# Kernel tuning notes

Measured on AMD Instinct MI355X. Metric: run time of the kernel, lower is better.

## Reference

```python
import jax, jax.numpy as jnp
import numpy as np

B, L, D, H, DH = 2, 2048, 768, 12, 3072
HD = D // H          # head dim = 64
EPS = 1e-6
SCALE = float(np.sqrt(HD))


def setup_inputs() -> dict:
    key = jax.random.key(0)
    ks = jax.random.split(key, 24)
    w = lambda k, shape: jax.random.normal(k, shape, jnp.float32) * 0.02
    # RoPE angles: [L, HD//2]
    inv_freq = 1.0 / (10000.0 ** (jnp.arange(HD // 2, dtype=jnp.float32) / (HD // 2)))
    ang = jnp.arange(L, dtype=jnp.float32)[:, None] * inv_freq[None, :]
    return {
        "x": jax.random.normal(ks[0], (B, L, D), jnp.float32),
        "c": jax.random.normal(ks[1], (B, D), jnp.float32),
        "freqs_cos": jnp.cos(ang),
        "freqs_sin": jnp.sin(ang),
        "W_q": w(ks[2], (D, D)), "W_k": w(ks[3], (D, D)),
        "W_v": w(ks[4], (D, D)), "W_o": w(ks[5], (D, D)),
        "cond_w1": w(ks[6], (D, DH)), "cond_b1": jnp.zeros((DH,), jnp.float32),
        "cond_w2": w(ks[7], (DH, D)), "cond_b2": jnp.zeros((D,), jnp.float32),
        "attn_norm_w": jnp.ones((D,), jnp.float32),
        "attn_alpha": w(ks[8], (D, D)), "attn_beta": w(ks[9], (D, D)),
        "attn_gamma": w(ks[10], (D, D)),
        "ffn_gate": w(ks[11], (D, DH)), "ffn_hidden": w(ks[12], (D, DH)),
        "ffn_out": w(ks[13], (DH, D)),
        "ffn_norm_w": jnp.ones((D,), jnp.float32),
        "ffn_beta": w(ks[14], (D, D)), "ffn_gamma": w(ks[15], (D, D)),
    }


def _rms_norm(x, w):
    return w * x * jax.lax.rsqrt(jnp.mean(x * x, axis=-1, keepdims=True) + EPS)


def _rope(x, cos, sin):
    # x: [b, n, l, hd]; complex pairs are consecutive (even, odd) lanes
    x0, x1 = x[..., 0::2], x[..., 1::2]
    c, s = cos[None, None], sin[None, None]          # [1,1,l,hd//2]
    r0 = x0 * c - x1 * s
    r1 = x0 * s + x1 * c
    return jnp.stack([r0, r1], axis=-1).reshape(x.shape)


def _attention(h, cos, sin, W_q, W_k, W_v, W_o):
    b, l, d = h.shape
    split = lambda y: y.reshape(b, l, H, HD).transpose(0, 2, 1, 3)  # b n l hd
    q = _rope(split(h @ W_q), cos, sin)
    k = _rope(split(h @ W_k), cos, sin)
    v = split(h @ W_v)
    scores = jnp.einsum("bnld,bnmd->bnlm", q, k) / SCALE
    attn = jax.nn.softmax(scores, axis=-1)
    o = jnp.einsum("bnlm,bnmd->bnld", attn, v)
    return o.transpose(0, 2, 1, 3).reshape(b, l, d) @ W_o


def reference(x, c, freqs_cos, freqs_sin, W_q, W_k, W_v, W_o,
              cond_w1, cond_b1, cond_w2, cond_b2,
              attn_norm_w, attn_alpha, attn_beta, attn_gamma,
              ffn_gate, ffn_hidden, ffn_out, ffn_norm_w, ffn_beta, ffn_gamma):
    # conditioning embedding
    c2 = jax.nn.silu(c @ cond_w1 + cond_b1) @ cond_w2 + cond_b2   # [b, d]
    mod = lambda W: (c2 @ W)[:, None]                              # [b, 1, d]
    # attention sub-block with AdaLN modulation + alpha gating
    h = _rms_norm(x, attn_norm_w) * mod(attn_gamma) + mod(attn_beta)
    x = x + _attention(h, freqs_cos, freqs_sin, W_q, W_k, W_v, W_o) * mod(attn_alpha)
    # SwiGLU FFN sub-block (original gates the residual by ffn_gamma, not alpha)
    h = _rms_norm(x, ffn_norm_w) * mod(ffn_gamma) + mod(ffn_beta)
    ff = (jax.nn.silu(h @ ffn_gate) * (h @ ffn_hidden)) @ ffn_out
    return x + ff * mod(ffn_gamma)
```

## Files before the change

kernel.cpp:

```cpp
#include <hip/hip_runtime.h>

typedef unsigned short u16;
typedef __attribute__((ext_vector_type(8))) short short8;
typedef __attribute__((ext_vector_type(4))) float f32x4;

#define L_SEQ 2048
#define NHEAD 12
#define KVB 128
#define QBLK 128

__device__ __forceinline__ u16 f2bf(float f) {
    union { float f; unsigned u; } x; x.f = f;
    unsigned r = x.u + 0x7fffu + ((x.u >> 16) & 1u);
    return (u16)(r >> 16);
}
__device__ __forceinline__ float bf2f(u16 u) {
    union { unsigned u; float f; } x; x.u = ((unsigned)u) << 16;
    return x.f;
}
__device__ __forceinline__ float silu_f(float x) { return x / (1.f + __expf(-x)); }

__device__ __forceinline__ void gload16(const u16* g, u16* l) {
    __builtin_amdgcn_global_load_lds(
        (const __attribute__((address_space(1))) void*)g,
        (__attribute__((address_space(3))) void*)l, 16, 0, 0);
}

__global__ __launch_bounds__(256) void transpose_all(
    const float* __restrict__ S0, const float* __restrict__ S1,
    const float* __restrict__ S2, const float* __restrict__ S3,
    const float* __restrict__ S4, const float* __restrict__ S5,
    const float* __restrict__ S6,
    u16* __restrict__ D0, u16* __restrict__ D1, u16* __restrict__ D2,
    u16* __restrict__ D3, u16* __restrict__ D4, u16* __restrict__ D5,
    u16* __restrict__ D6)
{
    int id = blockIdx.x;
    const float* W; u16* Wt; int K, N, local;
    if (id < 2304) {
        int sec = id / 576; local = id - sec * 576; K = 768; N = 768;
        W  = (sec == 0) ? S0 : (sec == 1) ? S1 : (sec == 2) ? S2 : S3;
        Wt = (sec == 0) ? D0 : (sec == 1) ? D1 : (sec == 2) ? D2 : D3;
    } else if (id < 6912) {
        int sec = (id - 2304) / 2304; local = (id - 2304) - sec * 2304; K = 768; N = 3072;
        W = sec ? S5 : S4; Wt = sec ? D5 : D4;
    } else {
        local = id - 6912; K = 3072; N = 768; W = S6; Wt = D6;
    }
    int nx = N >> 5;
    int n0 = (local % nx) * 32, k0 = (local / nx) * 32;
    __shared__ float t[32][33];
    int tx = threadIdx.x & 31, ty = threadIdx.x >> 5;
#pragma unroll
    for (int i = 0; i < 4; i++)
        t[ty + 8 * i][tx] = W[(size_t)(k0 + ty + 8 * i) * N + n0 + tx];
    __syncthreads();
#pragma unroll
    for (int i = 0; i < 4; i++)
        Wt[(size_t)(n0 + ty + 8 * i) * K + k0 + tx] = f2bf(t[tx][ty + 8 * i]);
}

__global__ __launch_bounds__(256) void cond_mlp1(
    const float* __restrict__ c, const float* __restrict__ w1, float* __restrict__ part)
{
    int j = blockIdx.x * 256 + threadIdx.x;
    int d0 = blockIdx.y * 96;
    float a0 = 0.f, a1 = 0.f;
    for (int d = d0; d < d0 + 96; ++d) {
        float w = w1[(size_t)d * 3072 + j];
        a0 += c[d] * w;
        a1 += c[768 + d] * w;
    }
    part[(size_t)(blockIdx.y * 2 + 0) * 3072 + j] = a0;
    part[(size_t)(blockIdx.y * 2 + 1) * 3072 + j] = a1;
}

__global__ __launch_bounds__(256) void cond_mlp2(
    const float* __restrict__ part, const float* __restrict__ b1,
    const float* __restrict__ w2, float* __restrict__ c2part)
{
    __shared__ float hid[2][384];
    const int tid = threadIdx.x;
    const int d0 = blockIdx.y * 384;
    for (int i = tid; i < 768; i += 256) {
        int b = i / 384, dd = i - b * 384;
        float s = b1[d0 + dd];
#pragma unroll
        for (int p = 0; p < 8; p++) s += part[(size_t)(p * 2 + b) * 3072 + d0 + dd];
        hid[b][dd] = silu_f(s);
    }
    __syncthreads();
    int jj = tid & 63, kc = tid >> 6;
    int j = blockIdx.x * 64 + jj;
    float a0 = 0.f, a1 = 0.f;
    for (int dd = kc * 96; dd < kc * 96 + 96; ++dd) {
        float w = w2[(size_t)(d0 + dd) * 768 + j];
        a0 += hid[0][dd] * w;
        a1 += hid[1][dd] * w;
    }
    __shared__ float r0[256], r1[256];
    r0[tid] = a0; r1[tid] = a1;
    __syncthreads();
    if (kc == 0) {
        a0 = r0[jj] + r0[64 + jj] + r0[128 + jj] + r0[192 + jj];
        a1 = r1[jj] + r1[64 + jj] + r1[128 + jj] + r1[192 + jj];
        c2part[(size_t)(blockIdx.y * 2 + 0) * 768 + j] = a0;
        c2part[(size_t)(blockIdx.y * 2 + 1) * 768 + j] = a1;
    }
}

__global__ __launch_bounds__(256) void mod_gemm(
    const float* __restrict__ c2part, const float* __restrict__ b2,
    const float* __restrict__ W0, const float* __restrict__ W1,
    const float* __restrict__ W2, const float* __restrict__ W3,
    const float* __restrict__ W4, float* __restrict__ out)
{
    __shared__ float c2s[2][768];
    const int tid = threadIdx.x;
    for (int i = tid; i < 1536; i += 256) {
        int b = i / 768, d = i - b * 768;
        float s = b2[d];
#pragma unroll
        for (int p = 0; p < 8; p++) s += c2part[(size_t)(p * 2 + b) * 768 + d];
        c2s[b][d] = s;
    }
    __syncthreads();
    int w = blockIdx.y;
    const float* W = (w == 0) ? W0 : (w == 1) ? W1 : (w == 2) ? W2 : (w == 3) ? W3 : W4;
    int jj = tid & 63, kc = tid >> 6;
    int j = blockIdx.x * 64 + jj;
    float a0 = 0.f, a1 = 0.f;
    for (int d = kc * 192; d < kc * 192 + 192; ++d) {
        float ww = W[(size_t)d * 768 + j];
        a0 += c2s[0][d] * ww;
        a1 += c2s[1][d] * ww;
    }
    __shared__ float r0[256], r1[256];
    r0[tid] = a0; r1[tid] = a1;
    __syncthreads();
    if (kc == 0) {
        a0 = r0[jj] + r0[64 + jj] + r0[128 + jj] + r0[192 + jj];
        a1 = r1[jj] + r1[64 + jj] + r1[128 + jj] + r1[192 + jj];
        out[(size_t)(w * 2 + 0) * 768 + j] = a0;
        out[(size_t)(w * 2 + 1) * 768 + j] = a1;
    }
}

__global__ __launch_bounds__(256) void rmsnorm_mod(
    const float* __restrict__ xin, const float* __restrict__ nw,
    const float* __restrict__ gamma, const float* __restrict__ beta,
    u16* __restrict__ hout)
{
    int row = blockIdx.x;
    int b = row >> 11;
    const float* xr = xin + (size_t)row * 768;
    int t = threadIdx.x;
    float v0 = xr[t], v1 = xr[t + 256], v2 = xr[t + 512];
    float ss = v0 * v0 + v1 * v1 + v2 * v2;
#pragma unroll
    for (int m = 1; m < 64; m <<= 1) ss += __shfl_xor(ss, m);
    __shared__ float red[4];
    if ((t & 63) == 0) red[t >> 6] = ss;
    __syncthreads();
    float tot = red[0] + red[1] + red[2] + red[3];
    float rr = rsqrtf(tot * (1.f / 768.f) + 1e-6f);
    u16* ho = hout + (size_t)row * 768;
    const float* g = gamma + (size_t)b * 768;
    const float* be = beta + (size_t)b * 768;
#pragma unroll
    for (int i = 0; i < 3; i++) {
        int col = t + i * 256;
        float v = (i == 0) ? v0 : (i == 1) ? v1 : v2;
        ho[col] = f2bf(v * rr * nw[col] * g[col] + be[col]);
    }
}

template<int BM, int WM, int MODE>
__global__ __launch_bounds__(256) void gemm_bf16(
    const u16* __restrict__ A, const u16* __restrict__ Bt,
    float* __restrict__ Cf, u16* __restrict__ Cb,
    const float* __restrict__ X, const float* __restrict__ coef,
    int M, int N, int K)
{
    constexpr int MR = WM / 16, NR = 4;
    __shared__ __align__(16) u16 As[2][BM * 32];
    __shared__ __align__(16) u16 Bs[2][128 * 32];
    const int tid = threadIdx.x;
    const int lane = tid & 63, wid = tid >> 6;
    const int lo = lane & 15, hi = lane >> 4;
    const int bm = blockIdx.x * BM, bn = blockIdx.y * 128;
    const int wrow = (wid >> 1) * WM, wcol = (wid & 1) * 64;

    f32x4 acc[MR][NR];
#pragma unroll
    for (int a = 0; a < MR; a++)
#pragma unroll
        for (int b = 0; b < NR; b++)
            acc[a][b] = (f32x4){0.f, 0.f, 0.f, 0.f};

    auto stage = [&](int buf, int k0) {
#pragma unroll
        for (int p = 0; p < BM / 64; p++) {
            int ch = tid + p * 256;
            gload16(A + (size_t)(bm + (ch >> 2)) * K + k0 + (ch & 3) * 8, &As[buf][ch * 8]);
        }
#pragma unroll
        for (int p = 0; p < 2; p++) {
            int ch = tid + p * 256;
            gload16(Bt + (size_t)(bn + (ch >> 2)) * K + k0 + (ch & 3) * 8, &Bs[buf][ch * 8]);
        }
    };

    stage(0, 0);
    int cur = 0;
    const int NT = K >> 5;
    for (int t = 0; t < NT; t++) {
        __syncthreads();
        if (t + 1 < NT) stage(cur ^ 1, (t + 1) * 32);
        short8 af[MR], bfr[NR];
#pragma unroll
        for (int mi = 0; mi < MR; mi++)
            af[mi] = *(const short8*)(&As[cur][(wrow + mi * 16 + lo) * 32 + hi * 8]);
#pragma unroll
        for (int nj = 0; nj < NR; nj++)
            bfr[nj] = *(const short8*)(&Bs[cur][(wcol + nj * 16 + lo) * 32 + hi * 8]);
        __builtin_amdgcn_s_setprio(1);
#pragma unroll
        for (int mi = 0; mi < MR; mi++)
#pragma unroll
            for (int nj = 0; nj < NR; nj++)
                acc[mi][nj] = __builtin_amdgcn_mfma_f32_16x16x32_bf16(af[mi], bfr[nj], acc[mi][nj], 0, 0, 0);
        __builtin_amdgcn_s_setprio(0);
        cur ^= 1;
    }
#pragma unroll
    for (int mi = 0; mi < MR; mi++)
#pragma unroll
        for (int nj = 0; nj < NR; nj++)
#pragma unroll
            for (int i = 0; i < 4; i++) {
                int row = bm + wrow + mi * 16 + hi * 4 + i;
                int col = bn + wcol + nj * 16 + lo;
                size_t idx = (size_t)row * N + col;
                float v = acc[mi][nj][i];
                if (MODE == 1) {
                    Cb[idx] = f2bf(v);
                } else {
                    int b = row >> 11;
                    Cf[idx] = X[idx] + v * coef[(size_t)b * N + col];
                }
            }
}

__global__ __launch_bounds__(256) void gemm_ffn1(
    const u16* __restrict__ A, const u16* __restrict__ Gt, const u16* __restrict__ Ht,
    u16* __restrict__ ff, int M, int N, int K)
{
    __shared__ __align__(16) u16 As[2][128 * 32];
    __shared__ __align__(16) u16 Gs[2][64 * 32];
    __shared__ __align__(16) u16 Hs[2][64 * 32];
    const int tid = threadIdx.x;
    const int lane = tid & 63, wid = tid >> 6;
    const int lo = lane & 15, hi = lane >> 4;
    const int bm = blockIdx.x * 128, bn = blockIdx.y * 64;
    const int wrow = (wid >> 1) * 64, wcol = (wid & 1) * 32;

    f32x4 ag[4][2], ah[4][2];
#pragma unroll
    for (int a = 0; a < 4; a++)
#pragma unroll
        for (int b = 0; b < 2; b++) {
            ag[a][b] = (f32x4){0.f, 0.f, 0.f, 0.f};
            ah[a][b] = (f32x4){0.f, 0.f, 0.f, 0.f};
        }

    auto stage = [&](int buf, int k0) {
#pragma unroll
        for (int p = 0; p < 2; p++) {
            int ch = tid + p * 256;
            gload16(A + (size_t)(bm + (ch >> 2)) * K + k0 + (ch & 3) * 8, &As[buf][ch * 8]);
        }
        {
            int ch = tid;
            gload16(Gt + (size_t)(bn + (ch >> 2)) * K + k0 + (ch & 3) * 8, &Gs[buf][ch * 8]);
            gload16(Ht + (size_t)(bn + (ch >> 2)) * K + k0 + (ch & 3) * 8, &Hs[buf][ch * 8]);
        }
    };

    stage(0, 0);
    int cur = 0;
    const int NT = K >> 5;
    for (int t = 0; t < NT; t++) {
        __syncthreads();
        if (t + 1 < NT) stage(cur ^ 1, (t + 1) * 32);
        short8 af[4], gf[2], hf[2];
#pragma unroll
        for (int mi = 0; mi < 4; mi++)
            af[mi] = *(const short8*)(&As[cur][(wrow + mi * 16 + lo) * 32 + hi * 8]);
#pragma unroll
        for (int nj = 0; nj < 2; nj++) {
            gf[nj] = *(const short8*)(&Gs[cur][(wcol + nj * 16 + lo) * 32 + hi * 8]);
            hf[nj] = *(const short8*)(&Hs[cur][(wcol + nj * 16 + lo) * 32 + hi * 8]);
        }
        __builtin_amdgcn_s_setprio(1);
#pragma unroll
        for (int mi = 0; mi < 4; mi++)
#pragma unroll
            for (int nj = 0; nj < 2; nj++) {
                ag[mi][nj] = __builtin_amdgcn_mfma_f32_16x16x32_bf16(af[mi], gf[nj], ag[mi][nj], 0, 0, 0);
                ah[mi][nj] = __builtin_amdgcn_mfma_f32_16x16x32_bf16(af[mi], hf[nj], ah[mi][nj], 0, 0, 0);
            }
        __builtin_amdgcn_s_setprio(0);
        cur ^= 1;
    }
#pragma unroll
    for (int mi = 0; mi < 4; mi++)
#pragma unroll
        for (int nj = 0; nj < 2; nj++)
#pragma unroll
            for (int i = 0; i < 4; i++) {
                int row = bm + wrow + mi * 16 + hi * 4 + i;
                int col = bn + wcol + nj * 16 + lo;
                ff[(size_t)row * N + col] = f2bf(silu_f(ag[mi][nj][i]) * ah[mi][nj][i]);
            }
}

__global__ __launch_bounds__(256) void rope_reshape(
    const u16* __restrict__ qr, const u16* __restrict__ kr, const u16* __restrict__ vr,
    const float* __restrict__ fc, const float* __restrict__ fs,
    u16* __restrict__ qo, u16* __restrict__ ko, u16* __restrict__ vt)
{
    const float QSCALE = 0.125f * 1.44269504f;
    __shared__ u16 Vl[64 * 64];
    const int tid = threadIdx.x;
    const int bh = blockIdx.y, lt = blockIdx.x;
    const int b = bh / NHEAD, h = bh % NHEAD;
    const int l0 = lt * 64;
    const int lrow = tid >> 2, ch = tid & 3;

    const size_t srow = ((size_t)(b * L_SEQ + l0 + lrow)) * 2304 + h * 64 + ch * 16;
    const size_t drow = ((size_t)(bh * L_SEQ + l0 + lrow)) * 64 + ch * 16;

    float cs[8], sn[8];
#pragma unroll
    for (int i = 0; i < 8; i++) {
        cs[i] = fc[(l0 + lrow) * 32 + ch * 8 + i];
        sn[i] = fs[(l0 + lrow) * 32 + ch * 8 + i];
    }
    union { int4 v4[2]; u16 s[16]; } iv, ov;
    iv.v4[0] = *(const int4*)(qr + srow); iv.v4[1] = *(const int4*)(qr + srow + 8);
#pragma unroll
    for (int i = 0; i < 8; i++) {
        float x0 = bf2f(iv.s[2 * i]), x1 = bf2f(iv.s[2 * i + 1]);
        ov.s[2 * i]     = f2bf((x0 * cs[i] - x1 * sn[i]) * QSCALE);
        ov.s[2 * i + 1] = f2bf((x0 * sn[i] + x1 * cs[i]) * QSCALE);
    }
    *(int4*)(qo + drow) = ov.v4[0]; *(int4*)(qo + drow + 8) = ov.v4[1];
    iv.v4[0] = *(const int4*)(kr + srow); iv.v4[1] = *(const int4*)(kr + srow + 8);
#pragma unroll
    for (int i = 0; i < 8; i++) {
        float x0 = bf2f(iv.s[2 * i]), x1 = bf2f(iv.s[2 * i + 1]);
        ov.s[2 * i]     = f2bf(x0 * cs[i] - x1 * sn[i]);
        ov.s[2 * i + 1] = f2bf(x0 * sn[i] + x1 * cs[i]);
    }
    *(int4*)(ko + drow) = ov.v4[0]; *(int4*)(ko + drow + 8) = ov.v4[1];
    iv.v4[0] = *(const int4*)(vr + srow); iv.v4[1] = *(const int4*)(vr + srow + 8);
#pragma unroll
    for (int e = 0; e < 16; e++) {
        int d = ch * 16 + e;
        Vl[d * 64 + (lrow ^ (((d >> 3) & 7) << 3))] = iv.s[e];
    }
    __syncthreads();
    const int d = tid >> 2;
    const int key = ((d >> 3) & 7) << 3;
    int4 o0 = *(const int4*)(&Vl[d * 64 + ((ch * 16) ^ key)]);
    int4 o1 = *(const int4*)(&Vl[d * 64 + ((ch * 16 + 8) ^ key)]);
    u16* vd = vt + ((size_t)bh * 64 + d) * L_SEQ + l0 + ch * 16;
    *(int4*)(vd) = o0; *(int4*)(vd + 8) = o1;
}

__global__ __launch_bounds__(512) void attn_fwd(
    const u16* __restrict__ q, const u16* __restrict__ k, const u16* __restrict__ vt,
    u16* __restrict__ outp)
{
    __shared__ __align__(16) u16 Kb[KVB * 64];
    __shared__ __align__(16) u16 Vb[64 * KVB];
    __shared__ __align__(16) u16 Ps[8][16 * KVB];
    const int tid = threadIdx.x;
    const int lane = tid & 63, wid = tid >> 6;
    const int lo = lane & 15, hi = lane >> 4;
    const int lid = blockIdx.x;
    const int xcd = lid & 7, li = lid >> 3;
    const int bh = xcd * 3 + (li >> 4);
    const int qt = li & 15;
    const int b = bh / NHEAD, h = bh % NHEAD;
    const int q0 = qt * QBLK + wid * 16;
    const u16* qb = q + ((size_t)bh * L_SEQ + q0) * 64;
    const u16* kbase = k + (size_t)bh * L_SEQ * 64;
    const u16* vbase = vt + (size_t)bh * 64 * L_SEQ;

    short8 qa0 = *(const short8*)(qb + lo * 64 + hi * 8);
    short8 qa1 = *(const short8*)(qb + lo * 64 + 32 + hi * 8);

    f32x4 oacc[4];
#pragma unroll
    for (int dt = 0; dt < 4; dt++) oacc[dt] = (f32x4){0.f, 0.f, 0.f, 0.f};
    float m_ = -1e30f, ls = 0.f;

    const int rk = tid >> 3, gk = tid & 7;
    const u16* ka = kbase + (size_t)rk * 64 + ((gk ^ (rk & 7)) * 8);
    const int rv = tid >> 4, gv = tid & 15;
    const u16* va = vbase + (size_t)rv * L_SEQ + ((gv ^ (rv & 15)) * 8);
    u16* kdst = &Kb[tid * 8];
    u16* vdst = &Vb[tid * 8];

    int4 kr0, kr1, vr0, vr1;
    kr0 = *(const int4*)(ka);
    kr1 = *(const int4*)(ka + 4096);
    vr0 = *(const int4*)(va);
    vr1 = *(const int4*)(va + 65536);

    const int NT = L_SEQ / KVB;
    u16* pw = &Ps[wid][0];
    const int pkey = lo << 3;
    for (int t = 0; t < NT; t++) {
        __syncthreads();
        *(int4*)(kdst)        = kr0;
        *(int4*)(kdst + 4096) = kr1;
        *(int4*)(vdst)        = vr0;
        *(int4*)(vdst + 4096) = vr1;
        __syncthreads();
        if (t + 1 < NT) {
            int kv0 = (t + 1) * KVB;
            const u16* kan = ka + (size_t)kv0 * 64;
            const u16* van = va + kv0;
            kr0 = *(const int4*)(kan);
            kr1 = *(const int4*)(kan + 4096);
            vr0 = *(const int4*)(van);
            vr1 = *(const int4*)(van + 65536);
        }
        f32x4 s[8];
#pragma unroll
        for (int nt = 0; nt < 8; nt++) {
            int kr_ = nt * 16 + lo;
            const u16* kp = &Kb[kr_ * 64];
            int key = (kr_ & 7) << 3;
            short8 kf0 = *(const short8*)(kp + ((hi * 8) ^ key));
            short8 kf1 = *(const short8*)(kp + ((32 + hi * 8) ^ key));
            __builtin_amdgcn_s_setprio(1);
            f32x4 z = (f32x4){0.f, 0.f, 0.f, 0.f};
            z = __builtin_amdgcn_mfma_f32_16x16x32_bf16(kf0, qa0, z, 0, 0, 0);
            s[nt] = __builtin_amdgcn_mfma_f32_16x16x32_bf16(kf1, qa1, s[nt] = z, 0, 0, 0);
            __builtin_amdgcn_s_setprio(0);
        }
        float t0 = fmaxf(fmaxf(s[0][0], s[0][1]), fmaxf(s[0][2], s[0][3]));
        float t1 = fmaxf(fmaxf(s[1][0], s[1][1]), fmaxf(s[1][2], s[1][3]));
        float t2 = fmaxf(fmaxf(s[2][0], s[2][1]), fmaxf(s[2][2], s[2][3]));
        float t3 = fmaxf(fmaxf(s[3][0], s[3][1]), fmaxf(s[3][2], s[3][3]));
        float t4 = fmaxf(fmaxf(s[4][0], s[4][1]), fmaxf(s[4][2], s[4][3]));
        float t5 = fmaxf(fmaxf(s[5][0], s[5][1]), fmaxf(s[5][2], s[5][3]));
        float t6 = fmaxf(fmaxf(s[6][0], s[6][1]), fmaxf(s[6][2], s[6][3]));
        float t7 = fmaxf(fmaxf(s[7][0], s[7][1]), fmaxf(s[7][2], s[7][3]));
        float pmax = fmaxf(fmaxf(fmaxf(t0, t1), fmaxf(t2, t3)),
                           fmaxf(fmaxf(t4, t5), fmaxf(t6, t7)));
        pmax = fmaxf(pmax, __shfl_xor(pmax, 16));
        pmax = fmaxf(pmax, __shfl_xor(pmax, 32));
        if (!__all(pmax - m_ <= 8.f)) {
            float mn = fmaxf(m_, pmax);
            float al = exp2f(m_ - mn);
            m_ = mn;
            ls *= al;
#pragma unroll
            for (int dt = 0; dt < 4; dt++) oacc[dt] *= al;
        }
        float rsA = 0.f, rsB = 0.f, rsC = 0.f, rsD = 0.f;
#pragma unroll
        for (int nt = 0; nt < 8; nt++) {
            float p0 = exp2f(s[nt][0] - m_);
            float p1 = exp2f(s[nt][1] - m_);
            float p2 = exp2f(s[nt][2] - m_);
            float p3 = exp2f(s[nt][3] - m_);
            s[nt][0] = p0; s[nt][1] = p1; s[nt][2] = p2; s[nt][3] = p3;
            rsA += p0; rsB += p1; rsC += p2; rsD += p3;
        }
        ls += (rsA + rsB) + (rsC + rsD);
#pragma unroll
        for (int nt = 0; nt < 8; nt++) {
            unsigned w0, w1;
            asm("v_cvt_pk_bf16_f32 %0, %1, %2" : "=v"(w0) : "v"(s[nt][0]), "v"(s[nt][1]));
            asm("v_cvt_pk_bf16_f32 %0, %1, %2" : "=v"(w1) : "v"(s[nt][2]), "v"(s[nt][3]));
            uint2 pk2; pk2.x = w0; pk2.y = w1;
            *(uint2*)(pw + lo * KVB + ((nt * 16 + hi * 4) ^ pkey)) = pk2;
        }
        short8 pa0 = *(const short8*)(pw + lo * KVB + ((0 * 32 + hi * 8) ^ pkey));
        short8 pa1 = *(const short8*)(pw + lo * KVB + ((1 * 32 + hi * 8) ^ pkey));
        short8 pa2 = *(const short8*)(pw + lo * KVB + ((2 * 32 + hi * 8) ^ pkey));
        short8 pa3 = *(const short8*)(pw + lo * KVB + ((3 * 32 + hi * 8) ^ pkey));
#pragma unroll
        for (int dt = 0; dt < 4; dt++) {
            int vr_ = dt * 16 + lo;
            const u16* vp = &Vb[vr_ * KVB];
            int vkey = (vr_ & 15) << 3;
            short8 vf0 = *(const short8*)(vp + ((0 * 32 + hi * 8) ^ vkey));
            short8 vf1 = *(const short8*)(vp + ((1 * 32 + hi * 8) ^ vkey));
            short8 vf2 = *(const short8*)(vp + ((2 * 32 + hi * 8) ^ vkey));
            short8 vf3 = *(const short8*)(vp + ((3 * 32 + hi * 8) ^ vkey));
            __builtin_amdgcn_s_setprio(1);
            oacc[dt] = __builtin_amdgcn_mfma_f32_16x16x32_bf16(vf0, pa0, oacc[dt], 0, 0, 0);
            oacc[dt] = __builtin_amdgcn_mfma_f32_16x16x32_bf16(vf1, pa1, oacc[dt], 0, 0, 0);
            oacc[dt] = __builtin_amdgcn_mfma_f32_16x16x32_bf16(vf2, pa2, oacc[dt], 0, 0, 0);
            oacc[dt] = __builtin_amdgcn_mfma_f32_16x16x32_bf16(vf3, pa3, oacc[dt], 0, 0, 0);
            __builtin_amdgcn_s_setprio(0);
        }
    }
    ls += __shfl_xor(ls, 16);
    ls += __shfl_xor(ls, 32);
    float inv = 1.f / ls;
    int qrow = q0 + lo;
    u16* orow = outp + ((size_t)(b * L_SEQ + qrow)) * 768 + h * 64;
#pragma unroll
    for (int dt = 0; dt < 4; dt++) {
        unsigned w0, w1;
        float o0 = oacc[dt][0] * inv, o1 = oacc[dt][1] * inv;
        float o2 = oacc[dt][2] * inv, o3 = oacc[dt][3] * inv;
        asm("v_cvt_pk_bf16_f32 %0, %1, %2" : "=v"(w0) : "v"(o0), "v"(o1));
        asm("v_cvt_pk_bf16_f32 %0, %1, %2" : "=v"(w1) : "v"(o2), "v"(o3));
        uint2 pk2; pk2.x = w0; pk2.y = w1;
        *(uint2*)(orow + dt * 16 + hi * 4) = pk2;
    }
}

extern "C" void kernel_launch(void* const* d_in, const int* in_sizes, int n_in,
                              void* d_out, int out_size, void* d_ws, size_t ws_size,
                              hipStream_t stream)
{
    const float* x      = (const float*)d_in[0];
    const float* c      = (const float*)d_in[1];
    const float* fcos   = (const float*)d_in[2];
    const float* fsin   = (const float*)d_in[3];
    const float* Wq     = (const float*)d_in[4];
    const float* Wk     = (const float*)d_in[5];
    const float* Wv     = (const float*)d_in[6];
    const float* Wo     = (const float*)d_in[7];
    const float* cw1    = (const float*)d_in[8];
    const float* cb1    = (const float*)d_in[9];
    const float* cw2    = (const float*)d_in[10];
    const float* cb2    = (const float*)d_in[11];
    const float* anw    = (const float*)d_in[12];
    const float* Walpha = (const float*)d_in[13];
    const float* Wbeta  = (const float*)d_in[14];
    const float* Wgamma = (const float*)d_in[15];
    const float* Wgate  = (const float*)d_in[16];
    const float* Whid   = (const float*)d_in[17];
    const float* Wout   = (const float*)d_in[18];
    const float* fnw    = (const float*)d_in[19];
    const float* Wbetaf = (const float*)d_in[20];
    const float* Wgammaf= (const float*)d_in[21];

    const int M = 4096;
    char* ws = (char*)d_ws;
    size_t off = 0;
    auto alloc = [&](size_t bytes) -> char* {
        char* p = ws + off;
        off += (bytes + 255) & ~(size_t)255;
        return p;
    };
    u16* wq_t   = (u16*)alloc((size_t)768 * 768 * 2);
    u16* wk_t   = (u16*)alloc((size_t)768 * 768 * 2);
    u16* wv_t   = (u16*)alloc((size_t)768 * 768 * 2);
    u16* wo_t   = (u16*)alloc((size_t)768 * 768 * 2);
    u16* gate_t = (u16*)alloc((size_t)3072 * 768 * 2);
    u16* hid_t  = (u16*)alloc((size_t)3072 * 768 * 2);
    u16* out_t  = (u16*)alloc((size_t)768 * 3072 * 2);
    float* part1 = (float*)alloc((size_t)8 * 2 * 3072 * 4);
    float* part2 = (float*)alloc((size_t)8 * 2 * 768 * 4);
    float* mods = (float*)alloc(5 * 2 * 768 * 4);
    u16* hbuf   = (u16*)alloc((size_t)M * 768 * 2);
    u16* qkvraw = (u16*)alloc((size_t)M * 2304 * 2);
    u16* qrope  = (u16*)alloc((size_t)M * 768 * 2);
    u16* krope  = (u16*)alloc((size_t)M * 768 * 2);
    u16* vtb    = (u16*)alloc((size_t)M * 768 * 2);
    u16* attnh  = (u16*)alloc((size_t)M * 768 * 2);
    float* ybuf = (float*)alloc((size_t)M * 768 * 4);
    u16* ffbuf  = (u16*)alloc((size_t)M * 3072 * 2);

    transpose_all<<<9216, 256, 0, stream>>>(
        Wq, Wk, Wv, Wo, Wgate, Whid, Wout,
        wq_t, wk_t, wv_t, wo_t, gate_t, hid_t, out_t);

    cond_mlp1<<<dim3(12, 8), 256, 0, stream>>>(c, cw1, part1);
    cond_mlp2<<<dim3(12, 8), 256, 0, stream>>>(part1, cb1, cw2, part2);
    mod_gemm<<<dim3(12, 5), 256, 0, stream>>>(
        part2, cb2, Wgamma, Wbeta, Walpha, Wgammaf, Wbetaf, mods);

    rmsnorm_mod<<<M, 256, 0, stream>>>(x, anw, mods + 0 * 1536, mods + 1 * 1536, hbuf);

    gemm_bf16<128, 64, 1><<<dim3(32, 18, 1), 256, 0, stream>>>(
        hbuf, wq_t, nullptr, qkvraw, nullptr, nullptr, M, 2304, 768);

    rope_reshape<<<dim3(32, 24), 256, 0, stream>>>(
        qkvraw, qkvraw + 768, qkvraw + 1536,
        fcos, fsin, qrope, krope, vtb);

    attn_fwd<<<dim3(384), 512, 0, stream>>>(qrope, krope, vtb, attnh);

    gemm_bf16<64, 32, 2><<<dim3(64, 6, 1), 256, 0, stream>>>(
        attnh, wo_t, ybuf, nullptr, x, mods + 2 * 1536, M, 768, 768);

    rmsnorm_mod<<<M, 256, 0, stream>>>(ybuf, fnw, mods + 3 * 1536, mods + 4 * 1536, hbuf);

    gemm_ffn1<<<dim3(32, 48), 256, 0, stream>>>(
        hbuf, gate_t, hid_t, ffbuf, M, 3072, 768);

    gemm_bf16<64, 32, 2><<<dim3(64, 6, 1), 256, 0, stream>>>(
        ffbuf, out_t, (float*)d_out, nullptr, ybuf, mods + 3 * 1536, M, 768, 3072);
}
```

Baseline: 260.8 us.

## Fuse RoPE into QKV GEMM epilogue and use BK=64 swizzled LDS tiles

Moves the RoPE rotation, Q scaling and head reshape into the QKV GEMM epilogue, using a lane shuffle to pair even and odd columns. This removes the full qkvraw intermediate write and re-read, leaving a small kernel that only transposes V. All GEMMs also move from a K-tile of 32 to 64 with an XOR-swizzled LDS layout, halving the K-loop iterations and barriers and reducing bank conflicts. In exchange, LDS use per block doubles, which may lower occupancy, and the epilogue now does scattered 2-byte stores plus per-element cos/sin loads.

```diff
diff --git a/kernel.cpp b/kernel.cpp
--- a/kernel.cpp
+++ b/kernel.cpp
@@ -175,80 +175,183 @@
     }
 }
 
-template<int BM, int WM, int MODE>
-__global__ __launch_bounds__(256) void gemm_bf16(
+
+__global__ __launch_bounds__(256) void gemm_qkv_rope(
     const u16* __restrict__ A, const u16* __restrict__ Bt,
-    float* __restrict__ Cf, u16* __restrict__ Cb,
-    const float* __restrict__ X, const float* __restrict__ coef,
+    const float* __restrict__ fc, const float* __restrict__ fs,
+    u16* __restrict__ qo, u16* __restrict__ ko, u16* __restrict__ vraw,
     int M, int N, int K)
 {
-    constexpr int MR = WM / 16, NR = 4;
-    __shared__ __align__(16) u16 As[2][BM * 32];
-    __shared__ __align__(16) u16 Bs[2][128 * 32];
+    const float QSCALE = 0.125f * 1.44269504f;
+    __shared__ __align__(16) u16 As[2][128 * 64];
+    __shared__ __align__(16) u16 Bs[2][128 * 64];
     const int tid = threadIdx.x;
     const int lane = tid & 63, wid = tid >> 6;
     const int lo = lane & 15, hi = lane >> 4;
-    const int bm = blockIdx.x * BM, bn = blockIdx.y * 128;
-    const int wrow = (wid >> 1) * WM, wcol = (wid & 1) * 64;
-
-    f32x4 acc[MR][NR];
-#pragma unroll
-    for (int a = 0; a < MR; a++)
-#pragma unroll
-        for (int b = 0; b < NR; b++)
+    const int bm = blockIdx.x * 128, bn = blockIdx.y * 128;
+    const int wrow = (wid >> 1) * 64, wcol = (wid & 1) * 64;
+
+    f32x4 acc[4][4];
+#pragma unroll
+    for (int a = 0; a < 4; a++)
+#pragma unroll
+        for (int b = 0; b < 4; b++)
             acc[a][b] = (f32x4){0.f, 0.f, 0.f, 0.f};
 
     auto stage = [&](int buf, int k0) {
 #pragma unroll
-        for (int p = 0; p < BM / 64; p++) {
+        for (int p = 0; p < 4; p++) {
             int ch = tid + p * 256;
-            gload16(A + (size_t)(bm + (ch >> 2)) * K + k0 + (ch & 3) * 8, &As[buf][ch * 8]);
-        }
+            int r = ch >> 3, g = ch & 7;
+            gload16(A + (size_t)(bm + r) * K + k0 + ((g ^ (r & 7)) * 8), &As[buf][ch * 8]);
+        }
+#pragma unroll
+        for (int p = 0; p < 4; p++) {
+            int ch = tid + p * 256;
+            int r = ch >> 3, g = ch & 7;
+            gload16(Bt + (size_t)(bn + r) * K + k0 + ((g ^ (r & 7)) * 8), &Bs[buf][ch * 8]);
+        }
+    };
+
+    stage(0, 0);
+    int cur = 0;
+    const int NT = K >> 6;
+    for (int t = 0; t < NT; t++) {
+        __syncthreads();
+        if (t + 1 < NT) stage(cur ^ 1, (t + 1) * 64);
+        short8 af[4][2], bfr[4][2];
+#pragma unroll
+        for (int mi = 0; mi < 4; mi++) {
+            int r = wrow + mi * 16 + lo;
+#pragma unroll
+            for (int h = 0; h < 2; h++)
+                af[mi][h] = *(const short8*)(&As[cur][r * 64 + (((h * 4 + hi) ^ (r & 7)) * 8)]);
+        }
+#pragma unroll
+        for (int nj = 0; nj < 4; nj++) {
+            int r = wcol + nj * 16 + lo;
+#pragma unroll
+            for (int h = 0; h < 2; h++)
+                bfr[nj][h] = *(const short8*)(&Bs[cur][r * 64 + (((h * 4 + hi) ^ (r & 7)) * 8)]);
+        }
+        __builtin_amdgcn_s_setprio(1);
+#pragma unroll
+        for (int mi = 0; mi < 4; mi++)
+#pragma unroll
+            for (int nj = 0; nj < 4; nj++) {
+                acc[mi][nj] = __builtin_amdgcn_mfma_f32_16x16x32_bf16(af[mi][0], bfr[nj][0], acc[mi][nj], 0, 0, 0);
+                acc[mi][nj] = __builtin_amdgcn_mfma_f32_16x16x32_bf16(af[mi][1], bfr[nj][1], acc[mi][nj], 0, 0, 0);
+            }
+        __builtin_amdgcn_s_setprio(0);
+        cur ^= 1;
+    }
+    const int which = bn / 768;
+#pragma unroll
+    for (int mi = 0; mi < 4; mi++)
+#pragma unroll
+        for (int nj = 0; nj < 4; nj++)
+#pragma unroll
+            for (int i = 0; i < 4; i++) {
+                int row = bm + wrow + mi * 16 + hi * 4 + i;
+                int col = bn + wcol + nj * 16 + lo;
+                float v = acc[mi][nj][i];
+                if (which == 2) {
+                    vraw[(size_t)row * 768 + (col - 1536)] = f2bf(v);
+                } else {
+                    int within = col - which * 768;
+                    int h = within >> 6, d = within & 63;
+                    int l = row & (L_SEQ - 1), b = row >> 11;
+                    int dp = d >> 1;
+                    float cc = fc[l * 32 + dp], sn = fs[l * 32 + dp];
+                    float pv = __shfl_xor(v, 1);
+                    float r_;
+                    if ((lo & 1) == 0) r_ = v * cc - pv * sn;
+                    else               r_ = pv * sn + v * cc;
+                    if (which == 0) r_ *= QSCALE;
+                    u16* dst = (which == 0) ? qo : ko;
+                    dst[(((size_t)(b * NHEAD + h)) * L_SEQ + l) * 64 + d] = f2bf(r_);
+                }
+            }
+}
+
+__global__ __launch_bounds__(256) void gemm_res64(
+    const u16* __restrict__ A, const u16* __restrict__ Bt,
+    float* __restrict__ Cf, const float* __restrict__ X, const float* __restrict__ coef,
+    int M, int N, int K)
+{
+    __shared__ __align__(16) u16 As[2][64 * 64];
+    __shared__ __align__(16) u16 Bs[2][128 * 64];
+    const int tid = threadIdx.x;
+    const int lane = tid & 63, wid = tid >> 6;
+    const int lo = lane & 15, hi = lane >> 4;
+    const int bm = blockIdx.x * 64, bn = blockIdx.y * 128;
+    const int wrow = (wid >> 1) * 32, wcol = (wid & 1) * 64;
+
+    f32x4 acc[2][4];
+#pragma unroll
+    for (int a = 0; a < 2; a++)
+#pragma unroll
+        for (int b = 0; b < 4; b++)
+            acc[a][b] = (f32x4){0.f, 0.f, 0.f, 0.f};
+
+    auto stage = [&](int buf, int k0) {
 #pragma unroll
         for (int p = 0; p < 2; p++) {
             int ch = tid + p * 256;
-            gload16(Bt + (size_t)(bn + (ch >> 2)) * K + k0 + (ch & 3) * 8, &Bs[buf][ch * 8]);
+            int r = ch >> 3, g = ch & 7;
+            gload16(A + (size_t)(bm + r) * K + k0 + ((g ^ (r & 7)) * 8), &As[buf][ch * 8]);
+        }
+#pragma unroll
+        for (int p = 0; p < 4; p++) {
+            int ch = tid + p * 256;
+            int r = ch >> 3, g = ch & 7;
+            gload16(Bt + (size_t)(bn + r) * K + k0 + ((g ^ (r & 7)) * 8), &Bs[buf][ch * 8]);
         }
     };
 
     stage(0, 0);
     int cur = 0;
-    const int NT = K >> 5;
+    const int NT = K >> 6;
     for (int t = 0; t < NT; t++) {
         __syncthreads();
-        if (t + 1 < NT) stage(cur ^ 1, (t + 1) * 32);
-        short8 af[MR], bfr[NR];
-#pragma unroll
-        for (int mi = 0; mi < MR; mi++)
-            af[mi] = *(const short8*)(&As[cur][(wrow + mi * 16 + lo) * 32 + hi * 8]);
-#pragma unroll
-        for (int nj = 0; nj < NR; nj++)
-            bfr[nj] = *(const short8*)(&Bs[cur][(wcol + nj * 16 + lo) * 32 + hi * 8]);
+        if (t + 1 < NT) stage(cur ^ 1, (t + 1) * 64);
+        short8 af[2][2], bfr[4][2];
+#pragma unroll
+        for (int mi = 0; mi < 2; mi++) {
+            int r = wrow + mi * 16 + lo;
+#pragma unroll
+            for (int h = 0; h < 2; h++)
+                af[mi][h] = *(const short8*)(&As[cur][r * 64 + (((h * 4 + hi) ^ (r & 7)) * 8)]);
+        }
+#pragma unroll
+        for (int nj = 0; nj < 4; nj++) {
+            int r = wcol + nj * 16 + lo;
+#pragma unroll
+            for (int h = 0; h < 2; h++)
+                bfr[nj][h] = *(const short8*)(&Bs[cur][r * 64 + (((h * 4 + hi) ^ (r & 7)) * 8)]);
+        }
         __builtin_amdgcn_s_setprio(1);
 #pragma unroll
-        for (int mi = 0; mi < MR; mi++)
-#pragma unroll
-            for (int nj = 0; nj < NR; nj++)
-                acc[mi][nj] = __builtin_amdgcn_mfma_f32_16x16x32_bf16(af[mi], bfr[nj], acc[mi][nj], 0, 0, 0);
+        for (int mi = 0; mi < 2; mi++)
+#pragma unroll
+            for (int nj = 0; nj < 4; nj++) {
+                acc[mi][nj] = __builtin_amdgcn_mfma_f32_16x16x32_bf16(af[mi][0], bfr[nj][0], acc[mi][nj], 0, 0, 0);
+                acc[mi][nj] = __builtin_amdgcn_mfma_f32_16x16x32_bf16(af[mi][1], bfr[nj][1], acc[mi][nj], 0, 0, 0);
+            }
         __builtin_amdgcn_s_setprio(0);
         cur ^= 1;
     }
 #pragma unroll
-    for (int mi = 0; mi < MR; mi++)
-#pragma unroll
-        for (int nj = 0; nj < NR; nj++)
+    for (int mi = 0; mi < 2; mi++)
+#pragma unroll
+        for (int nj = 0; nj < 4; nj++)
 #pragma unroll
             for (int i = 0; i < 4; i++) {
                 int row = bm + wrow + mi * 16 + hi * 4 + i;
                 int col = bn + wcol + nj * 16 + lo;
                 size_t idx = (size_t)row * N + col;
-                float v = acc[mi][nj][i];
-                if (MODE == 1) {
-                    Cb[idx] = f2bf(v);
-                } else {
-                    int b = row >> 11;
-                    Cf[idx] = X[idx] + v * coef[(size_t)b * N + col];
-                }
+                int b = row >> 11;
+                Cf[idx] = X[idx] + acc[mi][nj][i] * coef[(size_t)b * N + col];
             }
 }
 
@@ -256,9 +359,9 @@
     const u16* __restrict__ A, const u16* __restrict__ Gt, const u16* __restrict__ Ht,
     u16* __restrict__ ff, int M, int N, int K)
 {
-    __shared__ __align__(16) u16 As[2][128 * 32];
-    __shared__ __align__(16) u16 Gs[2][64 * 32];
-    __shared__ __align__(16) u16 Hs[2][64 * 32];
+    __shared__ __align__(16) u16 As[2][128 * 64];
+    __shared__ __align__(16) u16 Gs[2][64 * 64];
+    __shared__ __align__(16) u16 Hs[2][64 * 64];
     const int tid = threadIdx.x;
     const int lane = tid & 63, wid = tid >> 6;
     const int lo = lane & 15, hi = lane >> 4;
@@ -276,39 +379,57 @@
 
     auto stage = [&](int buf, int k0) {
 #pragma unroll
+        for (int p = 0; p < 4; p++) {
+            int ch = tid + p * 256;
+            int r = ch >> 3, g = ch & 7;
+            gload16(A + (size_t)(bm + r) * K + k0 + ((g ^ (r & 7)) * 8), &As[buf][ch * 8]);
+        }
+#pragma unroll
         for (int p = 0; p < 2; p++) {
             int ch = tid + p * 256;
-            gload16(A + (size_t)(bm + (ch >> 2)) * K + k0 + (ch & 3) * 8, &As[buf][ch * 8]);
-        }
-        {
-            int ch = tid;
-            gload16(Gt + (size_t)(bn + (ch >> 2)) * K + k0 + (ch & 3) * 8, &Gs[buf][ch * 8]);
-            gload16(Ht + (size_t)(bn + (ch >> 2)) * K + k0 + (ch & 3) * 8, &Hs[buf][ch * 8]);
+            int r = ch >> 3, g = ch & 7;
+            gload16(Gt + (size_t)(bn + r) * K + k0 + ((g ^ (r & 7)) * 8), &Gs[buf][ch * 8]);
+        }
+#pragma unroll
+        for (int p = 0; p < 2; p++) {
+            int ch = tid + p * 256;
+            int r = ch >> 3, g = ch & 7;
+            gload16(Ht + (size_t)(bn + r) * K + k0 + ((g ^ (r & 7)) * 8), &Hs[buf][ch * 8]);
         }
     };
 
     stage(0, 0);
     int cur = 0;
-    const int NT = K >> 5;
+    const int NT = K >> 6;
     for (int t = 0; t < NT; t++) {
         __syncthreads();
-        if (t + 1 < NT) stage(cur ^ 1, (t + 1) * 32);
-        short8 af[4], gf[2], hf[2];
+        if (t + 1 < NT) stage(cur ^ 1, (t + 1) * 64);
+        short8 af[4][2], gf[2][2], hf[2][2];
+#pragma unroll
+        for (int mi = 0; mi < 4; mi++) {
+            int r = wrow + mi * 16 + lo;
+#pragma unroll
+            for (int h = 0; h < 2; h++)
+                af[mi][h] = *(const short8*)(&As[cur][r * 64 + (((h * 4 + hi) ^ (r & 7)) * 8)]);
+        }
+#pragma unroll
+        for (int nj = 0; nj < 2; nj++) {
+            int r = wcol + nj * 16 + lo;
+#pragma unroll
+            for (int h = 0; h < 2; h++) {
+                gf[nj][h] = *(const short8*)(&Gs[cur][r * 64 + (((h * 4 + hi) ^ (r & 7)) * 8)]);
+                hf[nj][h] = *(const short8*)(&Hs[cur][r * 64 + (((h * 4 + hi) ^ (r & 7)) * 8)]);
+            }
+        }
+        __builtin_amdgcn_s_setprio(1);
 #pragma unroll
         for (int mi = 0; mi < 4; mi++)
-            af[mi] = *(const short8*)(&As[cur][(wrow + mi * 16 + lo) * 32 + hi * 8]);
-#pragma unroll
-        for (int nj = 0; nj < 2; nj++) {
-            gf[nj] = *(const short8*)(&Gs[cur][(wcol + nj * 16 + lo) * 32 + hi * 8]);
-            hf[nj] = *(const short8*)(&Hs[cur][(wcol + nj * 16 + lo) * 32 + hi * 8]);
-        }
-        __builtin_amdgcn_s_setprio(1);
-#pragma unroll
-        for (int mi = 0; mi < 4; mi++)
 #pragma unroll
             for (int nj = 0; nj < 2; nj++) {
-                ag[mi][nj] = __builtin_amdgcn_mfma_f32_16x16x32_bf16(af[mi], gf[nj], ag[mi][nj], 0, 0, 0);
-                ah[mi][nj] = __builtin_amdgcn_mfma_f32_16x16x32_bf16(af[mi], hf[nj], ah[mi][nj], 0, 0, 0);
+                ag[mi][nj] = __builtin_amdgcn_mfma_f32_16x16x32_bf16(af[mi][0], gf[nj][0], ag[mi][nj], 0, 0, 0);
+                ag[mi][nj] = __builtin_amdgcn_mfma_f32_16x16x32_bf16(af[mi][1], gf[nj][1], ag[mi][nj], 0, 0, 0);
+                ah[mi][nj] = __builtin_amdgcn_mfma_f32_16x16x32_bf16(af[mi][0], hf[nj][0], ah[mi][nj], 0, 0, 0);
+                ah[mi][nj] = __builtin_amdgcn_mfma_f32_16x16x32_bf16(af[mi][1], hf[nj][1], ah[mi][nj], 0, 0, 0);
             }
         __builtin_amdgcn_s_setprio(0);
         cur ^= 1;
@@ -325,45 +446,17 @@
             }
 }
 
-__global__ __launch_bounds__(256) void rope_reshape(
-    const u16* __restrict__ qr, const u16* __restrict__ kr, const u16* __restrict__ vr,
-    const float* __restrict__ fc, const float* __restrict__ fs,
-    u16* __restrict__ qo, u16* __restrict__ ko, u16* __restrict__ vt)
-{
-    const float QSCALE = 0.125f * 1.44269504f;
+__global__ __launch_bounds__(256) void v_transpose(
+    const u16* __restrict__ vr, u16* __restrict__ vt)
+{
     __shared__ u16 Vl[64 * 64];
     const int tid = threadIdx.x;
     const int bh = blockIdx.y, lt = blockIdx.x;
     const int b = bh / NHEAD, h = bh % NHEAD;
     const int l0 = lt * 64;
     const int lrow = tid >> 2, ch = tid & 3;
-
-    const size_t srow = ((size_t)(b * L_SEQ + l0 + lrow)) * 2304 + h * 64 + ch * 16;
-    const size_t drow = ((size_t)(bh * L_SEQ + l0 + lrow)) * 64 + ch * 16;
-
-    float cs[8], sn[8];
-#pragma unroll
-    for (int i = 0; i < 8; i++) {
-        cs[i] = fc[(l0 + lrow) * 32 + ch * 8 + i];
-        sn[i] = fs[(l0 + lrow) * 32 + ch * 8 + i];
-    }
-    union { int4 v4[2]; u16 s[16]; } iv, ov;
-    iv.v4[0] = *(const int4*)(qr + srow); iv.v4[1] = *(const int4*)(qr + srow + 8);
-#pragma unroll
-    for (int i = 0; i < 8; i++) {
-        float x0 = bf2f(iv.s[2 * i]), x1 = bf2f(iv.s[2 * i + 1]);
-        ov.s[2 * i]     = f2bf((x0 * cs[i] - x1 * sn[i]) * QSCALE);
-        ov.s[2 * i + 1] = f2bf((x0 * sn[i] + x1 * cs[i]) * QSCALE);
-    }
-    *(int4*)(qo + drow) = ov.v4[0]; *(int4*)(qo + drow + 8) = ov.v4[1];
-    iv.v4[0] = *(const int4*)(kr + srow); iv.v4[1] = *(const int4*)(kr + srow + 8);
-#pragma unroll
-    for (int i = 0; i < 8; i++) {
-        float x0 = bf2f(iv.s[2 * i]), x1 = bf2f(iv.s[2 * i + 1]);
-        ov.s[2 * i]     = f2bf(x0 * cs[i] - x1 * sn[i]);
-        ov.s[2 * i + 1] = f2bf(x0 * sn[i] + x1 * cs[i]);
-    }
-    *(int4*)(ko + drow) = ov.v4[0]; *(int4*)(ko + drow + 8) = ov.v4[1];
+    const size_t srow = ((size_t)(b * L_SEQ + l0 + lrow)) * 768 + h * 64 + ch * 16;
+    union { int4 v4[2]; u16 s[16]; } iv;
     iv.v4[0] = *(const int4*)(vr + srow); iv.v4[1] = *(const int4*)(vr + srow + 8);
 #pragma unroll
     for (int e = 0; e < 16; e++) {
@@ -576,7 +669,7 @@
     float* part2 = (float*)alloc((size_t)8 * 2 * 768 * 4);
     float* mods = (float*)alloc(5 * 2 * 768 * 4);
     u16* hbuf   = (u16*)alloc((size_t)M * 768 * 2);
-    u16* qkvraw = (u16*)alloc((size_t)M * 2304 * 2);
+    u16* vraw   = (u16*)alloc((size_t)M * 768 * 2);
     u16* qrope  = (u16*)alloc((size_t)M * 768 * 2);
     u16* krope  = (u16*)alloc((size_t)M * 768 * 2);
     u16* vtb    = (u16*)alloc((size_t)M * 768 * 2);
@@ -595,23 +688,21 @@
 
     rmsnorm_mod<<<M, 256, 0, stream>>>(x, anw, mods + 0 * 1536, mods + 1 * 1536, hbuf);
 
-    gemm_bf16<128, 64, 1><<<dim3(32, 18, 1), 256, 0, stream>>>(
-        hbuf, wq_t, nullptr, qkvraw, nullptr, nullptr, M, 2304, 768);
-
-    rope_reshape<<<dim3(32, 24), 256, 0, stream>>>(
-        qkvraw, qkvraw + 768, qkvraw + 1536,
-        fcos, fsin, qrope, krope, vtb);
+    gemm_qkv_rope<<<dim3(32, 18), 256, 0, stream>>>(
+        hbuf, wq_t, fcos, fsin, qrope, krope, vraw, M, 2304, 768);
+
+    v_transpose<<<dim3(32, 24), 256, 0, stream>>>(vraw, vtb);
 
     attn_fwd<<<dim3(384), 512, 0, stream>>>(qrope, krope, vtb, attnh);
 
-    gemm_bf16<64, 32, 2><<<dim3(64, 6, 1), 256, 0, stream>>>(
-        attnh, wo_t, ybuf, nullptr, x, mods + 2 * 1536, M, 768, 768);
+    gemm_res64<<<dim3(64, 6), 256, 0, stream>>>(
+        attnh, wo_t, ybuf, x, mods + 2 * 1536, M, 768, 768);
 
     rmsnorm_mod<<<M, 256, 0, stream>>>(ybuf, fnw, mods + 3 * 1536, mods + 4 * 1536, hbuf);
 
     gemm_ffn1<<<dim3(32, 48), 256, 0, stream>>>(
         hbuf, gate_t, hid_t, ffbuf, M, 3072, 768);
 
-    gemm_bf16<64, 32, 2><<<dim3(64, 6, 1), 256, 0, stream>>>(
-        ffbuf, out_t, (float*)d_out, nullptr, ybuf, mods + 3 * 1536, M, 768, 3072);
-}
+    gemm_res64<<<dim3(64, 6), 256, 0, stream>>>(
+        ffbuf, out_t, (float*)d_out, ybuf, mods + 3 * 1536, M, 768, 3072);
+}
```

After: 252.0 us. 3.4% less time.
